# Kernel tuning notes

Hardware: AMD Instinct MI355X
Metric: run time of the kernel (lower is better)

Reference implementation:

```python
import jax, jax.numpy as jnp
import numpy as np

B, S, D, M = 16, 4096, 512, 2048


def setup_inputs() -> dict:
    key = jax.random.key(0)
    ks = jax.random.split(key, 10)
    init = lambda k, shape, fan: (jax.random.normal(k, shape, jnp.float32) / np.sqrt(fan).astype(np.float32))
    return {
        "x": jax.random.normal(ks[0], (B, S, D), jnp.float32),
        "W_qkv": init(ks[1], (D, 3 * D), D),
        "b_qkv": init(ks[2], (3 * D,), D),
        "W1": init(ks[3], (D, M), D),
        "b1": init(ks[4], (M,), D),
        "W2": init(ks[5], (M, M), M),
        "b2": init(ks[6], (M,), M),
        "W3": init(ks[7], (M, 1), M),
        "b3": init(ks[8], (1,), M),
    }


def reference(x, W_qkv, b_qkv, W1, b1, W2, b2, W3, b3):
    # qkv projection: [B,S,3D] -> split into q,k,v [B,S,D]
    qkv = jnp.einsum("bsd,de->bse", x, W_qkv) + b_qkv
    q, k, v = jnp.split(qkv, 3, axis=-1)
    # Only the last query row of causal SDPA is ever used; the last row of a
    # causal mask is fully unmasked, so this is plain attention of q[:, -1]
    # against all keys. scale=1.0 exactly as in the torch call.
    q_last = q[:, -1]                                  # [B, D]
    scores = jnp.einsum("bd,bsd->bs", q_last, k)       # [B, S], scale = 1.0
    attn = jax.nn.softmax(scores, axis=-1)
    sa_last = jnp.einsum("bs,bsd->bd", attn, v)        # [B, D]
    h = x[:, -1] + sa_last
    h = jax.nn.relu(h @ W1 + b1)
    h = jax.nn.relu(h @ W2 + b2)
    out = h @ W3 + b3                                  # [B, 1]
    return (out, q, k)
```

## Files before the change

kernel.cpp:

```cpp
#include <hip/hip_runtime.h>
#include <hip/hip_bf16.h>

#define B_  16
#define S_  4096
#define D_  512
#define M_  2048
#define ROWS (B_ * S_)
#define N3D  (3 * D_)

typedef __attribute__((ext_vector_type(8))) short bf16x8;
typedef __attribute__((ext_vector_type(4))) float f32x4;


__global__ __launch_bounds__(256) void cvt_x_kernel(const float* __restrict__ x,
                                                    __hip_bfloat16* __restrict__ xb) {
    long i = (long)blockIdx.x * 256 + threadIdx.x;
    const float4* x4 = (const float4*)x;
    float4 a = x4[2 * i], b = x4[2 * i + 1];
    union { __hip_bfloat16 h[8]; int4 v; } u;
    u.h[0] = __float2bfloat16(a.x); u.h[1] = __float2bfloat16(a.y);
    u.h[2] = __float2bfloat16(a.z); u.h[3] = __float2bfloat16(a.w);
    u.h[4] = __float2bfloat16(b.x); u.h[5] = __float2bfloat16(b.y);
    u.h[6] = __float2bfloat16(b.z); u.h[7] = __float2bfloat16(b.w);
    ((int4*)xb)[i] = u.v;
}

__global__ __launch_bounds__(256) void cvt_w_kernel(const float* __restrict__ w,
                                                    __hip_bfloat16* __restrict__ wt) {
    int idx = blockIdx.x * 256 + threadIdx.x;
    int n = idx >> 9, k = idx & 511;
    wt[idx] = __float2bfloat16(w[(long)k * N3D + n]);
}

__global__ __launch_bounds__(256) void gemm_qkv_kernel(
    const __hip_bfloat16* __restrict__ Xb,
    const __hip_bfloat16* __restrict__ Wt,
    const float* __restrict__ bias,
    float* __restrict__ qout, float* __restrict__ kout,
    __hip_bfloat16* __restrict__ vout)
{
    __shared__ __hip_bfloat16 As[128][40];
    __shared__ __hip_bfloat16 Bs[128][40];
    const int tid  = threadIdx.x;
    const int m0   = blockIdx.x * 128;
    const int n0   = blockIdx.y * 128;
    const int wave = tid >> 6, lane = tid & 63;
    const int wm   = (wave >> 1) * 64, wn = (wave & 1) * 64;
    const int quad = lane >> 4, l16 = lane & 15;

    const int srow  = tid >> 2;
    const int skcol = (tid & 3) * 8;

    f32x4 acc[4][4] = {};

    for (int k0 = 0; k0 < 512; k0 += 32) {
        int4 a0 = *(const int4*)(Xb + (long)(m0 + srow)      * 512 + k0 + skcol);
        int4 a1 = *(const int4*)(Xb + (long)(m0 + srow + 64) * 512 + k0 + skcol);
        int4 b0 = *(const int4*)(Wt + (long)(n0 + srow)      * 512 + k0 + skcol);
        int4 b1 = *(const int4*)(Wt + (long)(n0 + srow + 64) * 512 + k0 + skcol);
        __syncthreads();
        *(int4*)&As[srow][skcol]      = a0;
        *(int4*)&As[srow + 64][skcol] = a1;
        *(int4*)&Bs[srow][skcol]      = b0;
        *(int4*)&Bs[srow + 64][skcol] = b1;
        __syncthreads();

        bf16x8 af[4], bf[4];
        #pragma unroll
        for (int t = 0; t < 4; t++) {
            af[t] = *(const bf16x8*)&As[wm + t * 16 + l16][quad * 8];
            bf[t] = *(const bf16x8*)&Bs[wn + t * 16 + l16][quad * 8];
        }
        #pragma unroll
        for (int mt = 0; mt < 4; mt++)
            #pragma unroll
            for (int nt = 0; nt < 4; nt++)
                acc[mt][nt] = __builtin_amdgcn_mfma_f32_16x16x32_bf16(
                    af[mt], bf[nt], acc[mt][nt], 0, 0, 0);
    }

    #pragma unroll
    for (int mt = 0; mt < 4; mt++) {
        #pragma unroll
        for (int nt = 0; nt < 4; nt++) {
            int col = n0 + wn + nt * 16 + l16;
            float bcol = bias[col];
            #pragma unroll
            for (int r = 0; r < 4; r++) {
                int row = m0 + wm + mt * 16 + quad * 4 + r;
                float val = acc[mt][nt][r] + bcol;
                if (col < 512)        qout[(long)row * 512 + col]          = val;
                else if (col < 1024)  kout[(long)row * 512 + (col - 512)]  = val;
                else                  vout[(long)row * 512 + (col - 1024)] = __float2bfloat16(val);
            }
        }
    }
}


__global__ __launch_bounds__(256) void scores_kernel(
    const float* __restrict__ q, const float* __restrict__ k, float* __restrict__ sc)
{
    __shared__ float ql[512];
    int b = blockIdx.x, tid = threadIdx.x;
    const float* qrow = q + (long)(b * S_ + S_ - 1) * 512;
    ql[tid]       = qrow[tid];
    ql[tid + 256] = qrow[tid + 256];
    __syncthreads();
    int wave = tid >> 6, lane = tid & 63;
    int s0 = blockIdx.y * 64;
    float4 q1 = *(const float4*)&ql[lane * 8];
    float4 q2 = *(const float4*)&ql[lane * 8 + 4];
    for (int s = s0 + wave; s < s0 + 64; s += 4) {
        const float4* kr = (const float4*)(k + ((long)b * S_ + s) * 512);
        float4 x1 = kr[lane * 2], x2 = kr[lane * 2 + 1];
        float acc = x1.x * q1.x + x1.y * q1.y + x1.z * q1.z + x1.w * q1.w
                  + x2.x * q2.x + x2.y * q2.y + x2.z * q2.z + x2.w * q2.w;
        #pragma unroll
        for (int off = 32; off; off >>= 1) acc += __shfl_xor(acc, off);
        if (lane == 0) sc[(long)b * S_ + s] = acc;
    }
}

__global__ __launch_bounds__(256) void softmax_kernel(const float* __restrict__ sc,
                                                      float* __restrict__ attn)
{
    int b = blockIdx.x, tid = threadIdx.x;
    __shared__ float red[256];
    const float* row = sc + (long)b * S_;
    float mx = -1e30f;
    for (int s = tid; s < S_; s += 256) mx = fmaxf(mx, row[s]);
    red[tid] = mx; __syncthreads();
    for (int o = 128; o; o >>= 1) { if (tid < o) red[tid] = fmaxf(red[tid], red[tid + o]); __syncthreads(); }
    mx = red[0]; __syncthreads();
    float sum = 0.f;
    float* arow = attn + (long)b * S_;
    for (int s = tid; s < S_; s += 256) { float e = __expf(row[s] - mx); arow[s] = e; sum += e; }
    red[tid] = sum; __syncthreads();
    for (int o = 128; o; o >>= 1) { if (tid < o) red[tid] += red[tid + o]; __syncthreads(); }
    float inv = 1.0f / red[0];
    for (int s = tid; s < S_; s += 256) arow[s] *= inv;
}

__global__ __launch_bounds__(256) void h_init_kernel(const float* __restrict__ x,
                                                     float* __restrict__ h) {
    int i = blockIdx.x * 256 + threadIdx.x;
    int b = i >> 9, d = i & 511;
    h[i] = x[(long)(b * S_ + S_ - 1) * 512 + d];
}

__global__ __launch_bounds__(256) void sa_kernel(const __hip_bfloat16* __restrict__ v,
                                                 const float* __restrict__ attn,
                                                 float* __restrict__ h)
{
    int b  = blockIdx.x;
    int d0 = blockIdx.y * 128;
    int s0 = blockIdx.z * 512;
    int tid = threadIdx.x;
    int dt = (tid & 63) * 2;
    int sg = tid >> 6;
    float a0 = 0.f, a1 = 0.f;
    for (int s = s0 + sg; s < s0 + 512; s += 4) {
        float w = attn[(long)b * S_ + s];
        __hip_bfloat162 vv = *(const __hip_bfloat162*)(v + ((long)(b * S_ + s)) * 512 + d0 + dt);
        float2 vf = __bfloat1622float2(vv);
        a0 += w * vf.x; a1 += w * vf.y;
    }
    atomicAdd(&h[b * 512 + d0 + dt],     a0);
    atomicAdd(&h[b * 512 + d0 + dt + 1], a1);
}


__global__ __launch_bounds__(256) void mlp1_kernel(const float* __restrict__ h,
    const float* __restrict__ W1, const float* __restrict__ b1, float* __restrict__ h1)
{
    int b = blockIdx.x;
    int j = blockIdx.y * 256 + threadIdx.x;
    __shared__ float hs[512];
    hs[threadIdx.x]       = h[b * 512 + threadIdx.x];
    hs[threadIdx.x + 256] = h[b * 512 + threadIdx.x + 256];
    __syncthreads();
    float acc = 0.f;
    for (int k2 = 0; k2 < 512; k2++) acc += hs[k2] * W1[(long)k2 * M_ + j];
    acc += b1[j];
    h1[(long)b * M_ + j] = fmaxf(acc, 0.f);
}

__global__ __launch_bounds__(256) void mlp2_kernel(const float* __restrict__ h1,
    const float* __restrict__ W2, const float* __restrict__ b2, float* __restrict__ h2)
{
    int b = blockIdx.x;
    int j = blockIdx.y * 256 + threadIdx.x;
    __shared__ float hs[2048];
    for (int t = threadIdx.x; t < 2048; t += 256) hs[t] = h1[(long)b * M_ + t];
    __syncthreads();
    float acc = 0.f;
    for (int k2 = 0; k2 < 2048; k2++) acc += hs[k2] * W2[(long)k2 * M_ + j];
    acc += b2[j];
    h2[(long)b * M_ + j] = fmaxf(acc, 0.f);
}

__global__ __launch_bounds__(256) void mlp3_kernel(const float* __restrict__ h2,
    const float* __restrict__ W3, const float* __restrict__ b3, float* __restrict__ out)
{
    int b = blockIdx.x, tid = threadIdx.x;
    __shared__ float red[256];
    float acc = 0.f;
    for (int k2 = tid; k2 < 2048; k2 += 256) acc += h2[(long)b * M_ + k2] * W3[k2];
    red[tid] = acc; __syncthreads();
    for (int o = 128; o; o >>= 1) { if (tid < o) red[tid] += red[tid + o]; __syncthreads(); }
    if (tid == 0) out[b] = red[0] + b3[0];
}


extern "C" void kernel_launch(void* const* d_in, const int* in_sizes, int n_in,
                              void* d_out, int out_size, void* d_ws, size_t ws_size,
                              hipStream_t stream)
{
    const float* x    = (const float*)d_in[0];
    const float* Wqkv = (const float*)d_in[1];
    const float* bqkv = (const float*)d_in[2];
    const float* W1   = (const float*)d_in[3];
    const float* b1   = (const float*)d_in[4];
    const float* W2   = (const float*)d_in[5];
    const float* b2   = (const float*)d_in[6];
    const float* W3   = (const float*)d_in[7];
    const float* b3   = (const float*)d_in[8];

    float* out  = (float*)d_out;
    float* qout = out + 16;
    float* kout = qout + (size_t)ROWS * 512;

    char* ws = (char*)d_ws;
    size_t off = 0;
    auto alloc = [&](size_t bytes) -> char* {
        char* p = ws + off; off += (bytes + 255) & ~(size_t)255; return p;
    };
    __hip_bfloat16* Xb = (__hip_bfloat16*)alloc((size_t)ROWS * 512 * 2);
    __hip_bfloat16* Wt = (__hip_bfloat16*)alloc((size_t)N3D * 512 * 2);
    __hip_bfloat16* Vb = (__hip_bfloat16*)alloc((size_t)ROWS * 512 * 2);
    float* sc   = (float*)alloc((size_t)B_ * S_ * 4);
    float* attn = (float*)alloc((size_t)B_ * S_ * 4);
    float* h    = (float*)alloc((size_t)B_ * 512 * 4);
    float* h1   = (float*)alloc((size_t)B_ * M_ * 4);
    float* h2   = (float*)alloc((size_t)B_ * M_ * 4);

    hipLaunchKernelGGL(cvt_x_kernel,   dim3(ROWS * 512 / 8 / 256), dim3(256), 0, stream, x, Xb);
    hipLaunchKernelGGL(cvt_w_kernel,   dim3(N3D * 512 / 256),      dim3(256), 0, stream, Wqkv, Wt);
    hipLaunchKernelGGL(gemm_qkv_kernel, dim3(ROWS / 128, N3D / 128), dim3(256), 0, stream,
                       Xb, Wt, bqkv, qout, kout, Vb);
    hipLaunchKernelGGL(scores_kernel,  dim3(B_, 64), dim3(256), 0, stream, qout, kout, sc);
    hipLaunchKernelGGL(softmax_kernel, dim3(B_),     dim3(256), 0, stream, sc, attn);
    hipLaunchKernelGGL(h_init_kernel,  dim3(B_ * 512 / 256), dim3(256), 0, stream, x, h);
    hipLaunchKernelGGL(sa_kernel,      dim3(B_, 4, 8), dim3(256), 0, stream, Vb, attn, h);
    hipLaunchKernelGGL(mlp1_kernel,    dim3(B_, 8), dim3(256), 0, stream, h, W1, b1, h1);
    hipLaunchKernelGGL(mlp2_kernel,    dim3(B_, 8), dim3(256), 0, stream, h1, W2, b2, h2);
    hipLaunchKernelGGL(mlp3_kernel,    dim3(B_),    dim3(256), 0, stream, h2, W3, b3, out);
}
```

Before: 744.5 us.

## Use direct-to-LDS loads, coalesced GEMM epilogue, tiled transpose, split-K MLP

The QKV GEMM now fills its shared tiles with global_load_lds DMA loads instead of register staging, and drops the padded LDS layout. Its grid order is swapped so N varies fastest. The epilogue stages accumulators through swizzled shared memory so q/k/v are written as coalesced 16-byte vectors. The weight transpose uses a shared-memory tile, and the MLP layers split K across four waves with a shared reduction to get more blocks. The unpadded LDS layout may add bank conflicts on fragment reads, and the epilogue adds extra barriers.

```diff
diff --git a/kernel.cpp b/kernel.cpp
--- a/kernel.cpp
+++ b/kernel.cpp
@@ -10,6 +10,12 @@
 
 typedef __attribute__((ext_vector_type(8))) short bf16x8;
 typedef __attribute__((ext_vector_type(4))) float f32x4;
+
+__device__ __forceinline__ void load16(const void* g, void* l) {
+    __builtin_amdgcn_global_load_lds(
+        (const __attribute__((address_space(1))) void*)g,
+        (__attribute__((address_space(3))) void*)l, 16, 0, 0);
+}
 
 
 __global__ __launch_bounds__(256) void cvt_x_kernel(const float* __restrict__ x,
@@ -27,9 +33,17 @@
 
 __global__ __launch_bounds__(256) void cvt_w_kernel(const float* __restrict__ w,
                                                     __hip_bfloat16* __restrict__ wt) {
-    int idx = blockIdx.x * 256 + threadIdx.x;
-    int n = idx >> 9, k = idx & 511;
-    wt[idx] = __float2bfloat16(w[(long)k * N3D + n]);
+    __shared__ float t[64][65];
+    int nb = blockIdx.x * 64;
+    int kb = blockIdx.y * 64;
+    int tx = threadIdx.x & 63, ty = threadIdx.x >> 6;
+    #pragma unroll
+    for (int r = ty; r < 64; r += 4)
+        t[r][tx] = w[(long)(kb + r) * N3D + nb + tx];
+    __syncthreads();
+    #pragma unroll
+    for (int r = ty; r < 64; r += 4)
+        wt[(long)(nb + r) * 512 + kb + tx] = __float2bfloat16(t[tx][r]);
 }
 
 __global__ __launch_bounds__(256) void gemm_qkv_kernel(
@@ -39,37 +53,37 @@
     float* __restrict__ qout, float* __restrict__ kout,
     __hip_bfloat16* __restrict__ vout)
 {
-    __shared__ __hip_bfloat16 As[128][40];
-    __shared__ __hip_bfloat16 Bs[128][40];
+    __shared__ __hip_bfloat16 As[128 * 32];
+    __shared__ __hip_bfloat16 Bs[128 * 32];
     const int tid  = threadIdx.x;
-    const int m0   = blockIdx.x * 128;
-    const int n0   = blockIdx.y * 128;
+    const int n0   = blockIdx.x * 128;
+    const int m0   = blockIdx.y * 128;
     const int wave = tid >> 6, lane = tid & 63;
     const int wm   = (wave >> 1) * 64, wn = (wave & 1) * 64;
     const int quad = lane >> 4, l16 = lane & 15;
 
-    const int srow  = tid >> 2;
-    const int skcol = (tid & 3) * 8;
+    const int c0 = tid, c1 = tid + 256;
+    const int r0 = c0 >> 2, kc0 = (c0 & 3) * 8;
+    const int r1 = c1 >> 2, kc1 = (c1 & 3) * 8;
+
+    const __hip_bfloat16* Ab = Xb + (long)m0 * 512;
+    const __hip_bfloat16* Bb = Wt + (long)n0 * 512;
 
     f32x4 acc[4][4] = {};
 
     for (int k0 = 0; k0 < 512; k0 += 32) {
-        int4 a0 = *(const int4*)(Xb + (long)(m0 + srow)      * 512 + k0 + skcol);
-        int4 a1 = *(const int4*)(Xb + (long)(m0 + srow + 64) * 512 + k0 + skcol);
-        int4 b0 = *(const int4*)(Wt + (long)(n0 + srow)      * 512 + k0 + skcol);
-        int4 b1 = *(const int4*)(Wt + (long)(n0 + srow + 64) * 512 + k0 + skcol);
         __syncthreads();
-        *(int4*)&As[srow][skcol]      = a0;
-        *(int4*)&As[srow + 64][skcol] = a1;
-        *(int4*)&Bs[srow][skcol]      = b0;
-        *(int4*)&Bs[srow + 64][skcol] = b1;
+        load16(Ab + (long)r0 * 512 + k0 + kc0, (char*)As + c0 * 16);
+        load16(Ab + (long)r1 * 512 + k0 + kc1, (char*)As + c1 * 16);
+        load16(Bb + (long)r0 * 512 + k0 + kc0, (char*)Bs + c0 * 16);
+        load16(Bb + (long)r1 * 512 + k0 + kc1, (char*)Bs + c1 * 16);
         __syncthreads();
 
         bf16x8 af[4], bf[4];
         #pragma unroll
         for (int t = 0; t < 4; t++) {
-            af[t] = *(const bf16x8*)&As[wm + t * 16 + l16][quad * 8];
-            bf[t] = *(const bf16x8*)&Bs[wn + t * 16 + l16][quad * 8];
+            af[t] = *(const bf16x8*)&As[(wm + t * 16 + l16) * 32 + quad * 8];
+            bf[t] = *(const bf16x8*)&Bs[(wn + t * 16 + l16) * 32 + quad * 8];
         }
         #pragma unroll
         for (int mt = 0; mt < 4; mt++)
@@ -79,21 +93,42 @@
                     af[mt], bf[nt], acc[mt][nt], 0, 0, 0);
     }
 
+    __syncthreads();
+    float* ep = ((wave < 2) ? (float*)As : (float*)Bs) + (wave & 1) * 1024;
+    const int colblk = n0 + wn;
+
+    float bcol[4];
+    #pragma unroll
+    for (int nt = 0; nt < 4; nt++) bcol[nt] = bias[colblk + nt * 16 + l16];
+
     #pragma unroll
     for (int mt = 0; mt < 4; mt++) {
-        #pragma unroll
-        for (int nt = 0; nt < 4; nt++) {
-            int col = n0 + wn + nt * 16 + l16;
-            float bcol = bias[col];
+        const int sw = (quad & 1) * 16;
+        #pragma unroll
+        for (int nt = 0; nt < 4; nt++)
             #pragma unroll
-            for (int r = 0; r < 4; r++) {
-                int row = m0 + wm + mt * 16 + quad * 4 + r;
-                float val = acc[mt][nt][r] + bcol;
-                if (col < 512)        qout[(long)row * 512 + col]          = val;
-                else if (col < 1024)  kout[(long)row * 512 + (col - 512)]  = val;
-                else                  vout[(long)row * 512 + (col - 1024)] = __float2bfloat16(val);
+            for (int r = 0; r < 4; r++)
+                ep[(quad * 4 + r) * 64 + ((nt * 16 + l16) ^ sw)] = acc[mt][nt][r] + bcol[nt];
+        __syncthreads();
+        #pragma unroll
+        for (int p = 0; p < 4; p++) {
+            int rr  = p * 4 + (lane >> 4);
+            int cc  = (lane & 15) * 4;
+            f32x4 vals = *(const f32x4*)&ep[rr * 64 + (cc ^ ((p & 1) * 16))];
+            long row = m0 + wm + mt * 16 + rr;
+            int  col = colblk + cc;
+            if (colblk < 512) {
+                *(f32x4*)(qout + row * 512 + col) = vals;
+            } else if (colblk < 1024) {
+                *(f32x4*)(kout + row * 512 + (col - 512)) = vals;
+            } else {
+                union { __hip_bfloat16 h[4]; short4 s4; } u;
+                u.h[0] = __float2bfloat16(vals[0]); u.h[1] = __float2bfloat16(vals[1]);
+                u.h[2] = __float2bfloat16(vals[2]); u.h[3] = __float2bfloat16(vals[3]);
+                *(short4*)(vout + row * 512 + (col - 1024)) = u.s4;
             }
         }
+        if (mt < 3) __syncthreads();
     }
 }
 
@@ -174,30 +209,42 @@
 __global__ __launch_bounds__(256) void mlp1_kernel(const float* __restrict__ h,
     const float* __restrict__ W1, const float* __restrict__ b1, float* __restrict__ h1)
 {
-    int b = blockIdx.x;
-    int j = blockIdx.y * 256 + threadIdx.x;
+    int b = blockIdx.x, j0 = blockIdx.y * 64;
     __shared__ float hs[512];
-    hs[threadIdx.x]       = h[b * 512 + threadIdx.x];
-    hs[threadIdx.x + 256] = h[b * 512 + threadIdx.x + 256];
-    __syncthreads();
+    __shared__ float red[256];
+    int tid = threadIdx.x;
+    hs[tid]       = h[b * 512 + tid];
+    hs[tid + 256] = h[b * 512 + tid + 256];
+    __syncthreads();
+    int jj = tid & 63, kg = tid >> 6;
+    int j = j0 + jj;
     float acc = 0.f;
-    for (int k2 = 0; k2 < 512; k2++) acc += hs[k2] * W1[(long)k2 * M_ + j];
-    acc += b1[j];
-    h1[(long)b * M_ + j] = fmaxf(acc, 0.f);
+    for (int k2 = kg; k2 < 512; k2 += 4) acc += hs[k2] * W1[(long)k2 * M_ + j];
+    red[tid] = acc; __syncthreads();
+    if (kg == 0) {
+        float s = red[jj] + red[64 + jj] + red[128 + jj] + red[192 + jj] + b1[j];
+        h1[(long)b * M_ + j] = fmaxf(s, 0.f);
+    }
 }
 
 __global__ __launch_bounds__(256) void mlp2_kernel(const float* __restrict__ h1,
     const float* __restrict__ W2, const float* __restrict__ b2, float* __restrict__ h2)
 {
-    int b = blockIdx.x;
-    int j = blockIdx.y * 256 + threadIdx.x;
+    int b = blockIdx.x, j0 = blockIdx.y * 64;
     __shared__ float hs[2048];
-    for (int t = threadIdx.x; t < 2048; t += 256) hs[t] = h1[(long)b * M_ + t];
-    __syncthreads();
+    __shared__ float red[256];
+    int tid = threadIdx.x;
+    for (int t = tid; t < 2048; t += 256) hs[t] = h1[(long)b * M_ + t];
+    __syncthreads();
+    int jj = tid & 63, kg = tid >> 6;
+    int j = j0 + jj;
     float acc = 0.f;
-    for (int k2 = 0; k2 < 2048; k2++) acc += hs[k2] * W2[(long)k2 * M_ + j];
-    acc += b2[j];
-    h2[(long)b * M_ + j] = fmaxf(acc, 0.f);
+    for (int k2 = kg; k2 < 2048; k2 += 4) acc += hs[k2] * W2[(long)k2 * M_ + j];
+    red[tid] = acc; __syncthreads();
+    if (kg == 0) {
+        float s = red[jj] + red[64 + jj] + red[128 + jj] + red[192 + jj] + b2[j];
+        h2[(long)b * M_ + j] = fmaxf(s, 0.f);
+    }
 }
 
 __global__ __launch_bounds__(256) void mlp3_kernel(const float* __restrict__ h2,
@@ -246,14 +293,14 @@
     float* h2   = (float*)alloc((size_t)B_ * M_ * 4);
 
     hipLaunchKernelGGL(cvt_x_kernel,   dim3(ROWS * 512 / 8 / 256), dim3(256), 0, stream, x, Xb);
-    hipLaunchKernelGGL(cvt_w_kernel,   dim3(N3D * 512 / 256),      dim3(256), 0, stream, Wqkv, Wt);
-    hipLaunchKernelGGL(gemm_qkv_kernel, dim3(ROWS / 128, N3D / 128), dim3(256), 0, stream,
+    hipLaunchKernelGGL(cvt_w_kernel,   dim3(N3D / 64, 512 / 64),   dim3(256), 0, stream, Wqkv, Wt);
+    hipLaunchKernelGGL(gemm_qkv_kernel, dim3(N3D / 128, ROWS / 128), dim3(256), 0, stream,
                        Xb, Wt, bqkv, qout, kout, Vb);
     hipLaunchKernelGGL(scores_kernel,  dim3(B_, 64), dim3(256), 0, stream, qout, kout, sc);
     hipLaunchKernelGGL(softmax_kernel, dim3(B_),     dim3(256), 0, stream, sc, attn);
     hipLaunchKernelGGL(h_init_kernel,  dim3(B_ * 512 / 256), dim3(256), 0, stream, x, h);
     hipLaunchKernelGGL(sa_kernel,      dim3(B_, 4, 8), dim3(256), 0, stream, Vb, attn, h);
-    hipLaunchKernelGGL(mlp1_kernel,    dim3(B_, 8), dim3(256), 0, stream, h, W1, b1, h1);
-    hipLaunchKernelGGL(mlp2_kernel,    dim3(B_, 8), dim3(256), 0, stream, h1, W2, b2, h2);
-    hipLaunchKernelGGL(mlp3_kernel,    dim3(B_),    dim3(256), 0, stream, h2, W3, b3, out);
-}
+    hipLaunchKernelGGL(mlp1_kernel,    dim3(B_, 32), dim3(256), 0, stream, h, W1, b1, h1);
+    hipLaunchKernelGGL(mlp2_kernel,    dim3(B_, 32), dim3(256), 0, stream, h1, W2, b2, h2);
+    hipLaunchKernelGGL(mlp3_kernel,    dim3(B_),     dim3(256), 0, stream, h2, W3, b3, out);
+}
```

New measurement: 862.9 us. 15.9% more time.
